# Performance work log

Measured on AMD Instinct MI355X. Metric: run time of the kernel, lower is better.

The kernel has to match this reference:

```python
import jax, jax.numpy as jnp
import numpy as np

NUM_TOKENS = 2048
NUM_HEADS = 32
NUM_KV_HEADS = 8
HEAD_DIM = 128
ATTN_SCALE = 0.08838834764831845  # 1/sqrt(head_dim)


def setup_inputs() -> dict:
    key = jax.random.key(0)
    kq, kk, kv = jax.random.split(key, 3)
    q = jax.random.normal(kq, (NUM_TOKENS, NUM_HEADS, HEAD_DIM), dtype=jnp.float32)
    k = jax.random.normal(kk, (NUM_TOKENS, NUM_KV_HEADS, HEAD_DIM), dtype=jnp.float32)
    v = jax.random.normal(kv, (NUM_TOKENS, NUM_KV_HEADS, HEAD_DIM), dtype=jnp.float32)
    return {"q": q, "k": k, "v": v}


def reference(q, k, v):
    # Prefill path: all tokens attend causally; GQA expands kv heads.
    n_rep = NUM_HEADS // NUM_KV_HEADS
    k = jnp.repeat(k, n_rep, axis=1)  # (T, H, D)
    v = jnp.repeat(v, n_rep, axis=1)  # (T, H, D)
    # scores: (H, Tq, Tk)
    scores = jnp.einsum("thd,shd->hts", q, k) * ATTN_SCALE
    T = q.shape[0]
    causal = jnp.tril(jnp.ones((T, T), dtype=bool))  # (Tq, Tk)
    scores = jnp.where(causal[None, :, :], scores, -jnp.inf)
    weights = jax.nn.softmax(scores, axis=-1)
    out = jnp.einsum("hts,shd->thd", weights, v)  # (T, H, D)
    return out
```

## Files before the change

### kernel.cpp

```cpp
#include <hip/hip_runtime.h>

#define NT 2048
#define NH 32
#define NKV 8
#define HD 128
#define BM 128
#define BN 64
#define NQT (NT / BM)
#define SCALE_LOG2E 0.12754984003389239f
#define NEG_BIG -1.0e30f

typedef unsigned int   uint4v  __attribute__((ext_vector_type(4)));
typedef unsigned int   uint2v  __attribute__((ext_vector_type(2)));
typedef float          f32x4   __attribute__((ext_vector_type(4)));
typedef __bf16         bf16x8  __attribute__((ext_vector_type(8)));
typedef unsigned short u16;

#define PK 136
#define PV 72
#define PO 136

__device__ __forceinline__ float bf2f(unsigned u) {
  return __builtin_bit_cast(float, u << 16);
}
__device__ __forceinline__ unsigned f2bf(float f) {
  return (__builtin_bit_cast(unsigned, f) + 0x8000u) >> 16;
}
__device__ __forceinline__ unsigned pack_rn(float lo, float hi) {
  const unsigned ul = __builtin_bit_cast(unsigned, lo) + 0x8000u;
  const unsigned uh = __builtin_bit_cast(unsigned, hi) + 0x8000u;
  return __builtin_amdgcn_perm(ul, uh, 0x03020706u);
}

__global__ __launch_bounds__(256, 2)
void prep_kernel(const float* __restrict__ kg, const float* __restrict__ vg,
                 u16* __restrict__ wsk, u16* __restrict__ wsv) {
  __shared__ __align__(16) float lds_f[32 * 132];
  const int tid = threadIdx.x;
  const int hk  = (int)blockIdx.x >> 6;
  const int kv0 = ((int)blockIdx.x & 63) * 32;

#pragma unroll
  for (int r = 0; r < 4; ++r) {
    const int flat = r * 256 + tid;
    const int row = flat >> 5, q8 = flat & 31;
    const f32x4 a = *(const f32x4*)&kg[((kv0 + row) * NKV + hk) * HD + q8 * 4];
    uint2v pk;
    pk[0] = pack_rn(a[0], a[1]);
    pk[1] = pack_rn(a[2], a[3]);
    *(uint2v*)&wsk[(hk * NT + kv0 + row) * HD + q8 * 4] = pk;
  }
#pragma unroll
  for (int r = 0; r < 4; ++r) {
    const int flat = r * 256 + tid;
    const int row = flat >> 5, q8 = flat & 31;
    *(f32x4*)&lds_f[row * 132 + q8 * 4] =
        *(const f32x4*)&vg[((kv0 + row) * NKV + hk) * HD + q8 * 4];
  }
  __syncthreads();
  const int d = tid >> 1, half = tid & 1;
#pragma unroll
  for (int jj = 0; jj < 2; ++jj) {
    const int j = half * 2 + jj;
    uint4v outw;
#pragma unroll
    for (int e = 0; e < 4; ++e)
      outw[e] = pack_rn(lds_f[(j * 8 + 2 * e) * 132 + d],
                        lds_f[(j * 8 + 2 * e + 1) * 132 + d]);
    *(uint4v*)&wsv[(hk * HD + d) * NT + kv0 + j * 8] = outw;
  }
}

template <bool PRE>
__global__ __launch_bounds__(256, 2)
void fa_kernel(const float* __restrict__ qg, const float* __restrict__ kg,
               const float* __restrict__ vg, float* __restrict__ og,
               const u16* __restrict__ wsk, const u16* __restrict__ wsv) {
  __shared__ __align__(16) u16 lds_k[2][64 * PK];
  __shared__ __align__(16) u16 lds_v[2][HD * PV];

  const int tid  = threadIdx.x;
  const int lane = tid & 63;
  const int w    = tid >> 6;
  const int quad = lane >> 4;
  const int l16  = lane & 15;

  const int h  = blockIdx.x;
  const int hk = h >> 2;
  const int y  = (int)blockIdx.y;
  const int qt = (y < NQT / 2) ? (NQT - 1 - y) : (y - NQT / 2);
  const int q0  = qt * BM;
  const int q0w = q0 + w * 32;

  uint4v qf[2][4];
#pragma unroll
  for (int qn = 0; qn < 2; ++qn)
#pragma unroll
    for (int c = 0; c < 4; ++c) {
      const int row = q0w + qn * 16 + l16;
      const float* qp = &qg[(row * NH + h) * HD + c * 32 + quad * 8];
      const f32x4 a = *(const f32x4*)qp;
      const f32x4 b = *(const f32x4*)(qp + 4);
      uint4v rg;
      rg[0] = pack_rn(a[0] * SCALE_LOG2E, a[1] * SCALE_LOG2E);
      rg[1] = pack_rn(a[2] * SCALE_LOG2E, a[3] * SCALE_LOG2E);
      rg[2] = pack_rn(b[0] * SCALE_LOG2E, b[1] * SCALE_LOG2E);
      rg[3] = pack_rn(b[2] * SCALE_LOG2E, b[3] * SCALE_LOG2E);
      qf[qn][c] = rg;
    }

  f32x4 o[8][2];
#pragma unroll
  for (int nt = 0; nt < 8; ++nt)
#pragma unroll
    for (int qn = 0; qn < 2; ++qn)
#pragma unroll
      for (int r = 0; r < 4; ++r) o[nt][qn][r] = 0.f;

  float l_run[2] = {0.f, 0.f};

  const int njt = 2 * qt + 2;

  uint4v kreg[4], vreg[4];
  f32x4  kregf[4][2], vregf[4][2];

  auto stage_load = [&](int jt) {
    const int kvb = jt * BN;
    if (PRE) {
#pragma unroll
      for (int r = 0; r < 4; ++r) {
        const int flat = r * 256 + tid;
        kreg[r] = *(const uint4v*)&wsk[(hk * NT + kvb + (flat >> 4)) * HD + (flat & 15) * 8];
      }
#pragma unroll
      for (int r = 0; r < 4; ++r) {
        const int flat = r * 256 + tid;
        vreg[r] = *(const uint4v*)&wsv[(hk * HD + (flat >> 3)) * NT + kvb + (flat & 7) * 8];
      }
    } else {
#pragma unroll
      for (int r = 0; r < 4; ++r) {
        const int flat = r * 256 + tid;
        const float* kp = &kg[((kvb + (flat >> 4)) * NKV + hk) * HD + (flat & 15) * 8];
        kregf[r][0] = *(const f32x4*)kp;
        kregf[r][1] = *(const f32x4*)(kp + 4);
      }
#pragma unroll
      for (int r = 0; r < 4; ++r) {
        const int d0 = (r * 4 + w) * 8;
        const float* vp = &vg[((kvb + lane) * NKV + hk) * HD + d0];
        vregf[r][0] = *(const f32x4*)vp;
        vregf[r][1] = *(const f32x4*)(vp + 4);
      }
    }
  };
  auto stage_write = [&](int b) {
    if (PRE) {
#pragma unroll
      for (int r = 0; r < 4; ++r) {
        const int flat = r * 256 + tid;
        *(uint4v*)&lds_k[b][(flat >> 4) * PK + (flat & 15) * 8] = kreg[r];
      }
#pragma unroll
      for (int r = 0; r < 4; ++r) {
        const int flat = r * 256 + tid;
        *(uint4v*)&lds_v[b][(flat >> 3) * PV + (flat & 7) * 8] = vreg[r];
      }
    } else {
#pragma unroll
      for (int r = 0; r < 4; ++r) {
        const int flat = r * 256 + tid;
        uint4v pk;
        pk[0] = pack_rn(kregf[r][0][0], kregf[r][0][1]);
        pk[1] = pack_rn(kregf[r][0][2], kregf[r][0][3]);
        pk[2] = pack_rn(kregf[r][1][0], kregf[r][1][1]);
        pk[3] = pack_rn(kregf[r][1][2], kregf[r][1][3]);
        *(uint4v*)&lds_k[b][(flat >> 4) * PK + (flat & 15) * 8] = pk;
      }
#pragma unroll
      for (int r = 0; r < 4; ++r) {
        const int d0 = (r * 4 + w) * 8;
#pragma unroll
        for (int e = 0; e < 4; ++e) {
          lds_v[b][(d0 + e) * PV + lane]     = (u16)f2bf(vregf[r][0][e]);
          lds_v[b][(d0 + 4 + e) * PV + lane] = (u16)f2bf(vregf[r][1][e]);
        }
      }
    }
  };

  const int sl0 = (quad & 1) * 32 + l16;
  const int sl1 = sl0 + 16;
  const bool qlo = (quad < 2);

  stage_load(0);
  stage_write(0);
  __syncthreads();

  for (int jt = 0; jt < njt; ++jt) {
    const int kv0 = jt * BN;
    const int b   = jt & 1;
    const bool havenext = (jt + 1 < njt);
    if (havenext) stage_load(jt + 1);

    if (kv0 <= q0w + 31) {
      f32x4 s[4][2];
#pragma unroll
      for (int mt = 0; mt < 4; ++mt)
#pragma unroll
        for (int qn = 0; qn < 2; ++qn)
#pragma unroll
          for (int r = 0; r < 4; ++r) s[mt][qn][r] = 0.f;

#pragma unroll
      for (int c = 0; c < 4; ++c) {
#pragma unroll
        for (int mt = 0; mt < 4; ++mt) {
          const uint4v kf = *(uint4v*)&lds_k[b][(mt * 16 + l16) * PK + c * 32 + quad * 8];
#pragma unroll
          for (int qn = 0; qn < 2; ++qn)
            s[mt][qn] = __builtin_amdgcn_mfma_f32_16x16x32_bf16(
                __builtin_bit_cast(bf16x8, kf),
                __builtin_bit_cast(bf16x8, qf[qn][c]), s[mt][qn], 0, 0, 0);
        }
      }

      if (kv0 + BN - 1 > q0w) {
#pragma unroll
        for (int mt = 0; mt < 4; ++mt)
#pragma unroll
          for (int qn = 0; qn < 2; ++qn)
#pragma unroll
            for (int r = 0; r < 4; ++r) {
              const int kvgl = kv0 + mt * 16 + quad * 4 + r;
              const int qgl  = q0w + qn * 16 + l16;
              if (kvgl > qgl) s[mt][qn][r] = NEG_BIG;
            }
      }

      unsigned pk[4][2][2];
#pragma unroll
      for (int qn = 0; qn < 2; ++qn) {
        float ts = 0.f;
#pragma unroll
        for (int mt = 0; mt < 4; ++mt) {
#pragma unroll
          for (int r = 0; r < 4; ++r) {
            const float p = __builtin_amdgcn_exp2f(s[mt][qn][r]);
            s[mt][qn][r] = p;
            ts += p;
          }
          pk[mt][qn][0] = pack_rn(s[mt][qn][0], s[mt][qn][1]);
          pk[mt][qn][1] = pack_rn(s[mt][qn][2], s[mt][qn][3]);
        }
        l_run[qn] += ts;
      }

#pragma unroll
      for (int c2 = 0; c2 < 2; ++c2) {
        uint4v pf[2];
#pragma unroll
        for (int p = 0; p < 4; ++p) {
          const int sl = (p >> 1) ? sl1 : sl0;
#pragma unroll
          for (int qn = 0; qn < 2; ++qn) {
            const int vA = __shfl((int)pk[2 * c2][qn][p & 1], sl);
            const int vB = __shfl((int)pk[2 * c2 + 1][qn][p & 1], sl);
            pf[qn][p] = (unsigned)(qlo ? vA : vB);
          }
        }
#pragma unroll
        for (int nt = 0; nt < 8; ++nt) {
          const uint4v vf = *(uint4v*)&lds_v[b][(nt * 16 + l16) * PV + c2 * 32 + quad * 8];
#pragma unroll
          for (int qn = 0; qn < 2; ++qn)
            o[nt][qn] = __builtin_amdgcn_mfma_f32_16x16x32_bf16(
                __builtin_bit_cast(bf16x8, vf),
                __builtin_bit_cast(bf16x8, pf[qn]), o[nt][qn], 0, 0, 0);
        }
      }
    }

    if (havenext) {
      stage_write((jt + 1) & 1);
      __syncthreads();
    }
  }

  __syncthreads();

  u16* ob = ((u16*)lds_k) + w * 32 * PO;

#pragma unroll
  for (int qn = 0; qn < 2; ++qn) {
    float l = l_run[qn];
    l += __shfl_xor(l, 16);
    l += __shfl_xor(l, 32);
    const float inv = 1.0f / l;
#pragma unroll
    for (int nt = 0; nt < 8; ++nt) {
      uint2v ok2;
      ok2[0] = pack_rn(o[nt][qn][0] * inv, o[nt][qn][1] * inv);
      ok2[1] = pack_rn(o[nt][qn][2] * inv, o[nt][qn][3] * inv);
      *(uint2v*)&ob[(qn * 16 + l16) * PO + nt * 16 + quad * 4] = ok2;
    }
  }
  __asm__ __volatile__("s_waitcnt lgkmcnt(0)" ::: "memory");
#pragma unroll
  for (int rr = 0; rr < 8; ++rr) {
    const int idx = rr * 64 + lane;
    const int row = idx >> 4, ch = idx & 15;
    const uint4v ov = *(uint4v*)&ob[row * PO + ch * 8];
    f32x4 lo, hi;
    lo[0] = bf2f(ov[0] & 0xffffu); lo[1] = bf2f(ov[0] >> 16);
    lo[2] = bf2f(ov[1] & 0xffffu); lo[3] = bf2f(ov[1] >> 16);
    hi[0] = bf2f(ov[2] & 0xffffu); hi[1] = bf2f(ov[2] >> 16);
    hi[2] = bf2f(ov[3] & 0xffffu); hi[3] = bf2f(ov[3] >> 16);
    float* op = &og[((q0 + w * 32 + row) * NH + h) * HD + ch * 8];
    *(f32x4*)op       = lo;
    *(f32x4*)(op + 4) = hi;
  }
}

extern "C" void kernel_launch(void* const* d_in, const int* in_sizes, int n_in,
                              void* d_out, int out_size, void* d_ws, size_t ws_size,
                              hipStream_t stream) {
  (void)in_sizes; (void)n_in; (void)out_size;
  const float* q = (const float*)d_in[0];
  const float* k = (const float*)d_in[1];
  const float* v = (const float*)d_in[2];
  float* out = (float*)d_out;

  const size_t kv_bytes = (size_t)NKV * NT * HD * 2;
  dim3 grid(NH, NQT);
  if (ws_size >= 2 * kv_bytes) {
    u16* wsk = (u16*)d_ws;
    u16* wsv = wsk + (size_t)NKV * NT * HD;
    prep_kernel<<<dim3(NKV * 64), dim3(256), 0, stream>>>(k, v, wsk, wsv);
    fa_kernel<true><<<grid, dim3(256), 0, stream>>>(q, k, v, out, wsk, wsv);
  } else {
    fa_kernel<false><<<grid, dim3(256), 0, stream>>>(q, k, v, out, nullptr, nullptr);
  }
}
```

Baseline: 150.9 us.

## Pre-swizzle K/V tile images and DMA them directly into LDS

The prep kernel now writes each 64-row K/V tile as a contiguous, XOR-swizzled bf16 image, with V pre-permuted so the P operand needs no cross-lane shuffles. The attention kernel then copies tiles with global_load_lds straight into LDS, removing the register staging and the ds_write pass, and indexes the swizzled layout to avoid bank conflicts without padding. The P fragment is now taken directly from registers instead of through shuffles. The cost is a full vmcnt wait before each barrier and a more complex layout that must match between the two kernels.

```diff
diff --git a/kernel.cpp b/kernel.cpp
--- a/kernel.cpp
+++ b/kernel.cpp
@@ -16,8 +16,8 @@
 typedef __bf16         bf16x8  __attribute__((ext_vector_type(8)));
 typedef unsigned short u16;
 
-#define PK 136
-#define PV 72
+#define KIMG 8192
+#define VIMG 8192
 #define PO 136
 
 __device__ __forceinline__ float bf2f(unsigned u) {
@@ -32,42 +32,59 @@
   return __builtin_amdgcn_perm(ul, uh, 0x03020706u);
 }
 
+__device__ __forceinline__ void gload16(const u16* g, u16* l) {
+  __builtin_amdgcn_global_load_lds(
+      (const __attribute__((address_space(1))) unsigned int*)g,
+      (__attribute__((address_space(3))) unsigned int*)l, 16, 0, 0);
+}
+
 __global__ __launch_bounds__(256, 2)
 void prep_kernel(const float* __restrict__ kg, const float* __restrict__ vg,
                  u16* __restrict__ wsk, u16* __restrict__ wsv) {
-  __shared__ __align__(16) float lds_f[32 * 132];
+  __shared__ __align__(16) float lds_f[64 * 132];
   const int tid = threadIdx.x;
-  const int hk  = (int)blockIdx.x >> 6;
-  const int kv0 = ((int)blockIdx.x & 63) * 32;
-
-#pragma unroll
-  for (int r = 0; r < 4; ++r) {
-    const int flat = r * 256 + tid;
-    const int row = flat >> 5, q8 = flat & 31;
-    const f32x4 a = *(const f32x4*)&kg[((kv0 + row) * NKV + hk) * HD + q8 * 4];
-    uint2v pk;
+  const int hk  = (int)blockIdx.x >> 5;
+  const int t   = (int)blockIdx.x & 31;
+  const int kv0 = t * 64;
+  u16* __restrict__ kimg = wsk + (hk * 32 + t) * KIMG;
+  u16* __restrict__ vimg = wsv + (hk * 32 + t) * VIMG;
+
+#pragma unroll
+  for (int it = 0; it < 4; ++it) {
+    const int unit = it * 256 + tid;
+    const int kv = unit >> 4, ch = unit & 15;
+    const float* kp = &kg[((kv0 + kv) * NKV + hk) * HD + ch * 8];
+    const f32x4 a = *(const f32x4*)kp;
+    const f32x4 b = *(const f32x4*)(kp + 4);
+    uint4v pk;
     pk[0] = pack_rn(a[0], a[1]);
     pk[1] = pack_rn(a[2], a[3]);
-    *(uint2v*)&wsk[(hk * NT + kv0 + row) * HD + q8 * 4] = pk;
-  }
-#pragma unroll
-  for (int r = 0; r < 4; ++r) {
-    const int flat = r * 256 + tid;
-    const int row = flat >> 5, q8 = flat & 31;
-    *(f32x4*)&lds_f[row * 132 + q8 * 4] =
-        *(const f32x4*)&vg[((kv0 + row) * NKV + hk) * HD + q8 * 4];
+    pk[2] = pack_rn(b[0], b[1]);
+    pk[3] = pack_rn(b[2], b[3]);
+    *(uint4v*)&kimg[kv * 128 + ((ch * 8) ^ ((kv & 7) << 3))] = pk;
+  }
+
+#pragma unroll
+  for (int it = 0; it < 8; ++it) {
+    const int unit = it * 256 + tid;
+    const int kv = unit >> 5, c4 = unit & 31;
+    *(f32x4*)&lds_f[kv * 132 + c4 * 4] =
+        *(const f32x4*)&vg[((kv0 + kv) * NKV + hk) * HD + c4 * 4];
   }
   __syncthreads();
-  const int d = tid >> 1, half = tid & 1;
-#pragma unroll
-  for (int jj = 0; jj < 2; ++jj) {
-    const int j = half * 2 + jj;
-    uint4v outw;
-#pragma unroll
-    for (int e = 0; e < 4; ++e)
-      outw[e] = pack_rn(lds_f[(j * 8 + 2 * e) * 132 + d],
-                        lds_f[(j * 8 + 2 * e + 1) * 132 + d]);
-    *(uint4v*)&wsv[(hk * HD + d) * NT + kv0 + j * 8] = outw;
+
+#pragma unroll
+  for (int it = 0; it < 4; ++it) {
+    const int unit = it * 256 + tid;
+    const int d = unit >> 3, chunk = unit & 7;
+    const int c2 = chunk >> 2, qd = chunk & 3;
+    const int kb = c2 * 32 + qd * 4;
+    uint4v w;
+    w[0] = pack_rn(lds_f[(kb + 0) * 132 + d],  lds_f[(kb + 1) * 132 + d]);
+    w[1] = pack_rn(lds_f[(kb + 2) * 132 + d],  lds_f[(kb + 3) * 132 + d]);
+    w[2] = pack_rn(lds_f[(kb + 16) * 132 + d], lds_f[(kb + 17) * 132 + d]);
+    w[3] = pack_rn(lds_f[(kb + 18) * 132 + d], lds_f[(kb + 19) * 132 + d]);
+    *(uint4v*)&vimg[d * 64 + ((chunk * 8) ^ ((d & 7) << 3))] = w;
   }
 }
 
@@ -76,8 +93,7 @@
 void fa_kernel(const float* __restrict__ qg, const float* __restrict__ kg,
                const float* __restrict__ vg, float* __restrict__ og,
                const u16* __restrict__ wsk, const u16* __restrict__ wsv) {
-  __shared__ __align__(16) u16 lds_k[2][64 * PK];
-  __shared__ __align__(16) u16 lds_v[2][HD * PV];
+  __shared__ __align__(16) u16 lds[2][KIMG + VIMG];
 
   const int tid  = threadIdx.x;
   const int lane = tid & 63;
@@ -121,89 +137,99 @@
 
   const int njt = 2 * qt + 2;
 
-  uint4v kreg[4], vreg[4];
-  f32x4  kregf[4][2], vregf[4][2];
-
-  auto stage_load = [&](int jt) {
+  int kro[4], vro[2];
+#pragma unroll
+  for (int c = 0; c < 4; ++c)
+    kro[c] = l16 * 128 + ((c * 32 + quad * 8) ^ ((l16 & 7) << 3));
+#pragma unroll
+  for (int c2 = 0; c2 < 2; ++c2)
+    vro[c2] = l16 * 64 + ((c2 * 32 + quad * 8) ^ ((l16 & 7) << 3));
+
+  const int posl = (lane >> 5) * 32 + (((lane & 15) >> 2) << 3) +
+                   (((lane >> 4) & 1) << 2) + (lane & 3);
+
+  f32x4 kregf[4][2], vregf[4][2];
+
+  auto stage_dma = [&](int jt, int bb) {
+    const u16* ks = wsk + (hk * 32 + jt) * KIMG;
+    const u16* vs = wsv + (hk * 32 + jt) * VIMG;
+#pragma unroll
+    for (int r = 0; r < 4; ++r) {
+      const int fl = r * 256 + tid;
+      gload16(ks + fl * 8, &lds[bb][fl * 8]);
+    }
+#pragma unroll
+    for (int r = 0; r < 4; ++r) {
+      const int fl = r * 256 + tid;
+      gload16(vs + fl * 8, &lds[bb][KIMG + fl * 8]);
+    }
+  };
+
+  auto stage_load_f = [&](int jt) {
     const int kvb = jt * BN;
-    if (PRE) {
-#pragma unroll
-      for (int r = 0; r < 4; ++r) {
-        const int flat = r * 256 + tid;
-        kreg[r] = *(const uint4v*)&wsk[(hk * NT + kvb + (flat >> 4)) * HD + (flat & 15) * 8];
-      }
-#pragma unroll
-      for (int r = 0; r < 4; ++r) {
-        const int flat = r * 256 + tid;
-        vreg[r] = *(const uint4v*)&wsv[(hk * HD + (flat >> 3)) * NT + kvb + (flat & 7) * 8];
-      }
-    } else {
-#pragma unroll
-      for (int r = 0; r < 4; ++r) {
-        const int flat = r * 256 + tid;
-        const float* kp = &kg[((kvb + (flat >> 4)) * NKV + hk) * HD + (flat & 15) * 8];
-        kregf[r][0] = *(const f32x4*)kp;
-        kregf[r][1] = *(const f32x4*)(kp + 4);
-      }
-#pragma unroll
-      for (int r = 0; r < 4; ++r) {
-        const int d0 = (r * 4 + w) * 8;
-        const float* vp = &vg[((kvb + lane) * NKV + hk) * HD + d0];
-        vregf[r][0] = *(const f32x4*)vp;
-        vregf[r][1] = *(const f32x4*)(vp + 4);
-      }
+#pragma unroll
+    for (int r = 0; r < 4; ++r) {
+      const int flat = r * 256 + tid;
+      const float* kp = &kg[((kvb + (flat >> 4)) * NKV + hk) * HD + (flat & 15) * 8];
+      kregf[r][0] = *(const f32x4*)kp;
+      kregf[r][1] = *(const f32x4*)(kp + 4);
+    }
+#pragma unroll
+    for (int r = 0; r < 4; ++r) {
+      const int d0 = (r * 4 + w) * 8;
+      const float* vp = &vg[((kvb + lane) * NKV + hk) * HD + d0];
+      vregf[r][0] = *(const f32x4*)vp;
+      vregf[r][1] = *(const f32x4*)(vp + 4);
     }
   };
-  auto stage_write = [&](int b) {
-    if (PRE) {
-#pragma unroll
-      for (int r = 0; r < 4; ++r) {
-        const int flat = r * 256 + tid;
-        *(uint4v*)&lds_k[b][(flat >> 4) * PK + (flat & 15) * 8] = kreg[r];
-      }
-#pragma unroll
-      for (int r = 0; r < 4; ++r) {
-        const int flat = r * 256 + tid;
-        *(uint4v*)&lds_v[b][(flat >> 3) * PV + (flat & 7) * 8] = vreg[r];
-      }
-    } else {
-#pragma unroll
-      for (int r = 0; r < 4; ++r) {
-        const int flat = r * 256 + tid;
-        uint4v pk;
-        pk[0] = pack_rn(kregf[r][0][0], kregf[r][0][1]);
-        pk[1] = pack_rn(kregf[r][0][2], kregf[r][0][3]);
-        pk[2] = pack_rn(kregf[r][1][0], kregf[r][1][1]);
-        pk[3] = pack_rn(kregf[r][1][2], kregf[r][1][3]);
-        *(uint4v*)&lds_k[b][(flat >> 4) * PK + (flat & 15) * 8] = pk;
-      }
-#pragma unroll
-      for (int r = 0; r < 4; ++r) {
-        const int d0 = (r * 4 + w) * 8;
-#pragma unroll
-        for (int e = 0; e < 4; ++e) {
-          lds_v[b][(d0 + e) * PV + lane]     = (u16)f2bf(vregf[r][0][e]);
-          lds_v[b][(d0 + 4 + e) * PV + lane] = (u16)f2bf(vregf[r][1][e]);
-        }
+
+  auto stage_write_f = [&](int bb) {
+#pragma unroll
+    for (int r = 0; r < 4; ++r) {
+      const int flat = r * 256 + tid;
+      const int kv = flat >> 4, ch = flat & 15;
+      uint4v pk;
+      pk[0] = pack_rn(kregf[r][0][0], kregf[r][0][1]);
+      pk[1] = pack_rn(kregf[r][0][2], kregf[r][0][3]);
+      pk[2] = pack_rn(kregf[r][1][0], kregf[r][1][1]);
+      pk[3] = pack_rn(kregf[r][1][2], kregf[r][1][3]);
+      *(uint4v*)&lds[bb][kv * 128 + ((ch * 8) ^ ((kv & 7) << 3))] = pk;
+    }
+#pragma unroll
+    for (int r = 0; r < 4; ++r) {
+      const int d0 = (r * 4 + w) * 8;
+#pragma unroll
+      for (int e = 0; e < 8; ++e) {
+        const int d = d0 + e;
+        const float val = (e < 4) ? vregf[r][0][e] : vregf[r][1][e - 4];
+        lds[bb][KIMG + d * 64 + (posl ^ ((d & 7) << 3))] = (u16)f2bf(val);
       }
     }
   };
 
-  const int sl0 = (quad & 1) * 32 + l16;
-  const int sl1 = sl0 + 16;
-  const bool qlo = (quad < 2);
-
-  stage_load(0);
-  stage_write(0);
+  if (PRE) {
+    stage_dma(0, 0);
+    __asm__ __volatile__("s_waitcnt vmcnt(0)" ::: "memory");
+  } else {
+    stage_load_f(0);
+    stage_write_f(0);
+  }
   __syncthreads();
 
   for (int jt = 0; jt < njt; ++jt) {
     const int kv0 = jt * BN;
     const int b   = jt & 1;
     const bool havenext = (jt + 1 < njt);
-    if (havenext) stage_load(jt + 1);
+
+    if (havenext) {
+      if (PRE) stage_dma(jt + 1, b ^ 1);
+      else     stage_load_f(jt + 1);
+    }
 
     if (kv0 <= q0w + 31) {
+      const u16* lk = &lds[b][0];
+      const u16* lv = &lds[b][KIMG];
+
       f32x4 s[4][2];
 #pragma unroll
       for (int mt = 0; mt < 4; ++mt)
@@ -216,7 +242,7 @@
       for (int c = 0; c < 4; ++c) {
 #pragma unroll
         for (int mt = 0; mt < 4; ++mt) {
-          const uint4v kf = *(uint4v*)&lds_k[b][(mt * 16 + l16) * PK + c * 32 + quad * 8];
+          const uint4v kf = *(const uint4v*)&lk[mt * 2048 + kro[c]];
 #pragma unroll
           for (int qn = 0; qn < 2; ++qn)
             s[mt][qn] = __builtin_amdgcn_mfma_f32_16x16x32_bf16(
@@ -260,18 +286,15 @@
       for (int c2 = 0; c2 < 2; ++c2) {
         uint4v pf[2];
 #pragma unroll
-        for (int p = 0; p < 4; ++p) {
-          const int sl = (p >> 1) ? sl1 : sl0;
-#pragma unroll
-          for (int qn = 0; qn < 2; ++qn) {
-            const int vA = __shfl((int)pk[2 * c2][qn][p & 1], sl);
-            const int vB = __shfl((int)pk[2 * c2 + 1][qn][p & 1], sl);
-            pf[qn][p] = (unsigned)(qlo ? vA : vB);
-          }
+        for (int qn = 0; qn < 2; ++qn) {
+          pf[qn][0] = pk[2 * c2][qn][0];
+          pf[qn][1] = pk[2 * c2][qn][1];
+          pf[qn][2] = pk[2 * c2 + 1][qn][0];
+          pf[qn][3] = pk[2 * c2 + 1][qn][1];
         }
 #pragma unroll
         for (int nt = 0; nt < 8; ++nt) {
-          const uint4v vf = *(uint4v*)&lds_v[b][(nt * 16 + l16) * PV + c2 * 32 + quad * 8];
+          const uint4v vf = *(const uint4v*)&lv[nt * 1024 + vro[c2]];
 #pragma unroll
           for (int qn = 0; qn < 2; ++qn)
             o[nt][qn] = __builtin_amdgcn_mfma_f32_16x16x32_bf16(
@@ -282,14 +305,15 @@
     }
 
     if (havenext) {
-      stage_write((jt + 1) & 1);
+      if (!PRE) stage_write_f(b ^ 1);
+      if (PRE) __asm__ __volatile__("s_waitcnt vmcnt(0)" ::: "memory");
       __syncthreads();
     }
   }
 
   __syncthreads();
 
-  u16* ob = ((u16*)lds_k) + w * 32 * PO;
+  u16* ob = ((u16*)lds) + w * 32 * PO;
 
 #pragma unroll
   for (int qn = 0; qn < 2; ++qn) {
@@ -336,7 +360,7 @@
   if (ws_size >= 2 * kv_bytes) {
     u16* wsk = (u16*)d_ws;
     u16* wsv = wsk + (size_t)NKV * NT * HD;
-    prep_kernel<<<dim3(NKV * 64), dim3(256), 0, stream>>>(k, v, wsk, wsv);
+    prep_kernel<<<dim3(NKV * 32), dim3(256), 0, stream>>>(k, v, wsk, wsv);
     fa_kernel<true><<<grid, dim3(256), 0, stream>>>(q, k, v, out, wsk, wsv);
   } else {
     fa_kernel<false><<<grid, dim3(256), 0, stream>>>(q, k, v, out, nullptr, nullptr);
```

Result: faster. 137.5 us (-8.9%).
